# Kernel tuning notes

Hardware: AMD Instinct MI355X
Metric: run time of the kernel (lower is better)

The kernel has to match this reference:

```python
import jax, jax.numpy as jnp
import numpy as np

N_NODES = 50000
N_EDGES = 800000
D_IN = 128
D_OUT = 128
BN_EPS = 1e-5


def setup_inputs() -> dict:
    key = jax.random.key(0)
    ks = jax.random.split(key, 6)
    feat = jax.random.normal(ks[0], (N_NODES, D_IN), dtype=jnp.float32)
    src = jax.random.randint(ks[1], (N_EDGES,), 0, N_NODES, dtype=jnp.int32)
    dst = jax.random.randint(ks[2], (N_EDGES,), 0, N_NODES, dtype=jnp.int32)
    W = jax.random.normal(ks[3], (D_IN, D_OUT), dtype=jnp.float32) * (1.0 / np.sqrt(D_IN))
    b = jnp.zeros((D_OUT,), dtype=jnp.float32)
    a1 = jnp.full((1,), 0.25, dtype=jnp.float32)  # PReLU inside GraphConv
    gamma = jnp.ones((D_OUT,), dtype=jnp.float32)
    beta = jnp.zeros((D_OUT,), dtype=jnp.float32)
    a2 = jnp.full((1,), 0.25, dtype=jnp.float32)  # PReLU after BN
    return {"feat": feat, "src": src, "dst": dst, "W": W, "b": b,
            "a1": a1, "gamma": gamma, "beta": beta, "a2": a2}


def _prelu(x, a):
    return jnp.where(x >= 0, x, a * x)


def reference(feat, src, dst, W, b, a1, gamma, beta, a2):
    # Degrees (DGL clamps to min 1 to avoid inf norms)
    ones_e = jnp.ones((src.shape[0],), dtype=feat.dtype)
    out_deg = jnp.clip(jax.ops.segment_sum(ones_e, src, num_segments=N_NODES), 1.0)
    in_deg = jnp.clip(jax.ops.segment_sum(ones_e, dst, num_segments=N_NODES), 1.0)
    norm_src = jax.lax.rsqrt(out_deg)[:, None]   # [N,1]
    norm_dst = jax.lax.rsqrt(in_deg)[:, None]    # [N,1]

    # Dropout (eval mode -> identity), source normalization, projection
    h = (feat * norm_src) @ W                    # [N, D_OUT]
    # Gather-scatter neighbor aggregation (SpMM): sum over incoming edges
    msg = h[src]                                 # [E, D_OUT]
    agg = jax.ops.segment_sum(msg, dst, num_segments=N_NODES)  # [N, D_OUT]
    h = agg * norm_dst + b                       # dst normalization + bias
    h = _prelu(h, a1)                            # GraphConv activation

    # BatchNorm1d over node dimension (training-mode batch stats, biased var)
    mean = jnp.mean(h, axis=0)
    var = jnp.mean((h - mean) ** 2, axis=0)
    h = (h - mean) * jax.lax.rsqrt(var + BN_EPS) * gamma + beta

    return _prelu(h, a2)
```

## Files before the change

kernel.cpp:

```cpp
#include <hip/hip_runtime.h>
#include <hip/hip_bf16.h>

#define N_NODES 50000
#define N_EDGES 800000
#define D 128
#define BN_EPS 1e-5f
#define ELLW 64
#define PROJ_LDK 136
#define SPMM_BLOCKS 1564
#define PROJ_TILES 782

#define BINS 128
#define BIN_RANGE 391
#define BINCAP 8192
#define A_EPT 13
#define A_BLOCKS 256

typedef __attribute__((ext_vector_type(8))) short bf16x8;
typedef __attribute__((ext_vector_type(4))) float f32x4;

__device__ inline float bf_lo(unsigned u) { union { unsigned x; float f; } c; c.x = u << 16; return c.f; }
__device__ inline float bf_hi(unsigned u) { union { unsigned x; float f; } c; c.x = u & 0xffff0000u; return c.f; }
__device__ inline unsigned short f2bf(float f) {
    union { float f; unsigned u; } c; c.f = f;
    unsigned u = c.u;
    u += 0x7fff + ((u >> 16) & 1);
    return (unsigned short)(u >> 16);
}
__device__ inline unsigned cvt_pk_bf16(float lo, float hi) {
    unsigned r;
    asm("v_cvt_pk_bf16_f32 %0, %1, %2" : "=v"(r) : "v"(lo), "v"(hi));
    return r;
}

__global__ __launch_bounds__(256, 2) void bucket_proj_kernel(
        const int* __restrict__ src,
        const int* __restrict__ dst,
        int* __restrict__ gdbase,
        int* __restrict__ gsbase,
        unsigned* __restrict__ dbkt,
        unsigned short* __restrict__ sbkt,
        const float* __restrict__ feat,
        const float* __restrict__ W,
        unsigned short* __restrict__ h) {
    __shared__ int dcnt[BINS], scnt[BINS], dbase[BINS], sbase[BINS];
    __shared__ unsigned short Wt[D * PROJ_LDK];

    const int tid = threadIdx.x;

    if (blockIdx.x < A_BLOCKS) {
        if (tid < BINS) { dcnt[tid] = 0; scnt[tid] = 0; }
        __syncthreads();

        const int e0 = blockIdx.x * (256 * A_EPT) + tid;
        int s[A_EPT], t[A_EPT], dr[A_EPT], sr[A_EPT];
        #pragma unroll
        for (int k = 0; k < A_EPT; ++k) {
            int e = e0 + k * 256;
            if (e < N_EDGES) { s[k] = src[e]; t[k] = dst[e]; }
            else             { s[k] = -1;     t[k] = -1;     }
        }
        #pragma unroll
        for (int k = 0; k < A_EPT; ++k) {
            if (t[k] >= 0) dr[k] = atomicAdd(&dcnt[t[k] / BIN_RANGE], 1);
            if (s[k] >= 0) sr[k] = atomicAdd(&scnt[s[k] / BIN_RANGE], 1);
        }
        __syncthreads();
        if (tid < BINS) {
            dbase[tid] = atomicAdd(&gdbase[tid], dcnt[tid]);
            sbase[tid] = atomicAdd(&gsbase[tid], scnt[tid]);
        }
        __syncthreads();
        #pragma unroll
        for (int k = 0; k < A_EPT; ++k) {
            if (t[k] >= 0) {
                int bb = t[k] / BIN_RANGE;
                int p = dbase[bb] + dr[k];
                if (p < BINCAP)
                    dbkt[bb * BINCAP + p] = (unsigned)s[k] | ((unsigned)(t[k] - bb * BIN_RANGE) << 16);
            }
            if (s[k] >= 0) {
                int bb = s[k] / BIN_RANGE;
                int p = sbase[bb] + sr[k];
                if (p < BINCAP)
                    sbkt[bb * BINCAP + p] = (unsigned short)(s[k] - bb * BIN_RANGE);
            }
        }
    } else {
        const int tile = blockIdx.x - A_BLOCKS;
        const int wave = tid >> 6;
        const int lane = tid & 63;
        const int quad = lane >> 4;
        const int l16  = lane & 15;

        for (int idx = tid; idx < D * D; idx += 256) {
            int k = idx >> 7, d = idx & 127;
            Wt[d * PROJ_LDK + k] = f2bf(W[idx]);
        }
        __syncthreads();

        bf16x8 breg[8][4];
        #pragma unroll
        for (int dt = 0; dt < 8; ++dt)
            #pragma unroll
            for (int kk = 0; kk < 4; ++kk)
                breg[dt][kk] = *(const bf16x8*)&Wt[(dt * 16 + l16) * PROJ_LDK + kk * 32 + quad * 8];

        const int base = tile * 64;
        const int arow = base + wave * 16 + l16;
        const bool rok = arow < N_NODES;

        f32x4 acc[8];
        #pragma unroll
        for (int dt = 0; dt < 8; ++dt) acc[dt] = (f32x4){0.f, 0.f, 0.f, 0.f};

        #pragma unroll
        for (int kk = 0; kk < 4; ++kk) {
            bf16x8 af = (bf16x8){0, 0, 0, 0, 0, 0, 0, 0};
            if (rok) {
                const float4* fp = (const float4*)(feat + (size_t)arow * D + kk * 32 + quad * 8);
                float4 f0 = fp[0], f1 = fp[1];
                unsigned u0 = cvt_pk_bf16(f0.x, f0.y);
                unsigned u1 = cvt_pk_bf16(f0.z, f0.w);
                unsigned u2 = cvt_pk_bf16(f1.x, f1.y);
                unsigned u3 = cvt_pk_bf16(f1.z, f1.w);
                af[0] = (short)(u0 & 0xffff); af[1] = (short)(u0 >> 16);
                af[2] = (short)(u1 & 0xffff); af[3] = (short)(u1 >> 16);
                af[4] = (short)(u2 & 0xffff); af[5] = (short)(u2 >> 16);
                af[6] = (short)(u3 & 0xffff); af[7] = (short)(u3 >> 16);
            }
            #pragma unroll
            for (int dt = 0; dt < 8; ++dt)
                acc[dt] = __builtin_amdgcn_mfma_f32_16x16x32_bf16(af, breg[dt][kk], acc[dt], 0, 0, 0);
        }

        #pragma unroll
        for (int r = 0; r < 4; ++r) {
            int n = base + wave * 16 + quad * 4 + r;
            if (n < N_NODES) {
                unsigned short* hp = h + (size_t)n * D + l16;
                #pragma unroll
                for (int dt = 0; dt < 8; dt += 2) {
                    unsigned pk = cvt_pk_bf16(acc[dt][r], acc[dt + 1][r]);
                    hp[dt * 16]       = (unsigned short)(pk & 0xffff);
                    hp[(dt + 1) * 16] = (unsigned short)(pk >> 16);
                }
            }
        }
    }
}

__global__ __launch_bounds__(1024) void build_kernel(const int* __restrict__ gdbase,
                                                     const int* __restrict__ gsbase,
                                                     const unsigned* __restrict__ dbkt,
                                                     const unsigned short* __restrict__ sbkt,
                                                     unsigned short* __restrict__ ell,
                                                     int* __restrict__ cnt,
                                                     float* __restrict__ nsrc) {
    __shared__ int hist[BIN_RANGE];
    const int tid = threadIdx.x;
    const int bin = blockIdx.x & (BINS - 1);
    const int lo  = bin * BIN_RANGE;

    for (int i = tid; i < BIN_RANGE; i += 1024) hist[i] = 0;
    __syncthreads();

    if (blockIdx.x < BINS) {
        int count = gdbase[bin]; if (count > BINCAP) count = BINCAP;
        const unsigned* bkt = dbkt + bin * BINCAP;
        int i = tid;
        for (; i + 3072 < count; i += 4096) {
            unsigned e0 = bkt[i], e1 = bkt[i + 1024], e2 = bkt[i + 2048], e3 = bkt[i + 3072];
            int r0 = atomicAdd(&hist[e0 >> 16], 1);
            int r1 = atomicAdd(&hist[e1 >> 16], 1);
            int r2 = atomicAdd(&hist[e2 >> 16], 1);
            int r3 = atomicAdd(&hist[e3 >> 16], 1);
            if (r0 < ELLW) ell[(size_t)(lo + (e0 >> 16)) * ELLW + r0] = (unsigned short)(e0 & 0xffffu);
            if (r1 < ELLW) ell[(size_t)(lo + (e1 >> 16)) * ELLW + r1] = (unsigned short)(e1 & 0xffffu);
            if (r2 < ELLW) ell[(size_t)(lo + (e2 >> 16)) * ELLW + r2] = (unsigned short)(e2 & 0xffffu);
            if (r3 < ELLW) ell[(size_t)(lo + (e3 >> 16)) * ELLW + r3] = (unsigned short)(e3 & 0xffffu);
        }
        for (; i < count; i += 1024) {
            unsigned e = bkt[i];
            int r = atomicAdd(&hist[e >> 16], 1);
            if (r < ELLW) ell[(size_t)(lo + (e >> 16)) * ELLW + r] = (unsigned short)(e & 0xffffu);
        }
        __syncthreads();
        for (int j = tid; j < BIN_RANGE; j += 1024)
            if (lo + j < N_NODES) cnt[lo + j] = hist[j];
    } else {
        int count = gsbase[bin]; if (count > BINCAP) count = BINCAP;
        const unsigned short* bkt = sbkt + bin * BINCAP;
        int i = tid;
        for (; i + 3072 < count; i += 4096) {
            int v0 = bkt[i], v1 = bkt[i + 1024], v2 = bkt[i + 2048], v3 = bkt[i + 3072];
            atomicAdd(&hist[v0], 1); atomicAdd(&hist[v1], 1);
            atomicAdd(&hist[v2], 1); atomicAdd(&hist[v3], 1);
        }
        for (; i < count; i += 1024) atomicAdd(&hist[bkt[i]], 1);
        __syncthreads();
        for (int j = tid; j < BIN_RANGE; j += 1024)
            if (lo + j < N_NODES) {
                int dg = hist[j];
                nsrc[lo + j] = rsqrtf((float)(dg < 1 ? 1 : dg));
            }
    }
}

#define ACCA(v, ns) { accA[0] = fmaf(bf_lo((v).x), ns, accA[0]); accA[1] = fmaf(bf_hi((v).x), ns, accA[1]); \
                      accA[2] = fmaf(bf_lo((v).y), ns, accA[2]); accA[3] = fmaf(bf_hi((v).y), ns, accA[3]); \
                      accA[4] = fmaf(bf_lo((v).z), ns, accA[4]); accA[5] = fmaf(bf_hi((v).z), ns, accA[5]); \
                      accA[6] = fmaf(bf_lo((v).w), ns, accA[6]); accA[7] = fmaf(bf_hi((v).w), ns, accA[7]); }
#define ACCB(v, ns) { accB[0] = fmaf(bf_lo((v).x), ns, accB[0]); accB[1] = fmaf(bf_hi((v).x), ns, accB[1]); \
                      accB[2] = fmaf(bf_lo((v).y), ns, accB[2]); accB[3] = fmaf(bf_hi((v).y), ns, accB[3]); \
                      accB[4] = fmaf(bf_lo((v).z), ns, accB[4]); accB[5] = fmaf(bf_hi((v).z), ns, accB[5]); \
                      accB[6] = fmaf(bf_lo((v).w), ns, accB[6]); accB[7] = fmaf(bf_hi((v).w), ns, accB[7]); }
#define GA(sid) { int _s = (int)(sid); uint4 vv = *(const uint4*)(h + (size_t)_s * D + coff); \
                  float ns = nsrc[_s]; ACCA(vv, ns); }
#define GB(sid) { int _s = (int)(sid); uint4 vv = *(const uint4*)(h + (size_t)_s * D + coff); \
                  float ns = nsrc[_s]; ACCB(vv, ns); }

__global__ __launch_bounds__(256) void spmm_kernel(const int* __restrict__ cnt,
                                                   const float* __restrict__ nsrc,
                                                   const unsigned short* __restrict__ ell,
                                                   const unsigned short* __restrict__ h,
                                                   const float* __restrict__ b,
                                                   const float* __restrict__ a1,
                                                   unsigned short* __restrict__ h2,
                                                   float* __restrict__ bn_sum,
                                                   float* __restrict__ bn_sumsq) {
    const int tid  = threadIdx.x;
    const int l16  = tid & 15;
    const int slot = (blockIdx.x * 256 + tid) >> 4;
    const float alpha = a1[0];
    const size_t coff = (size_t)l16 * 8;

    float bias[8];
    #pragma unroll
    for (int j = 0; j < 8; ++j) bias[j] = b[l16 * 8 + j];

    float lsum[8] = {0,0,0,0,0,0,0,0};
    float lsq[8]  = {0,0,0,0,0,0,0,0};

    if (slot < N_NODES / 2) {
        const int n0 = slot * 2;
        const int n1 = n0 + 1;
        int dgA = cnt[n0], dgB = cnt[n1];
        int endA = (dgA < ELLW) ? dgA : ELLW;
        int endB = (dgB < ELLW) ? dgB : ELLW;
        const unsigned short* rowA = ell + (size_t)n0 * ELLW;
        const unsigned short* rowB = ell + (size_t)n1 * ELLW;

        float accA[8] = {0,0,0,0,0,0,0,0};
        float accB[8] = {0,0,0,0,0,0,0,0};
        int iA = 0, iB = 0;

        while (iA + 8 <= endA && iB + 8 <= endB) {
            uint4 ra = *(const uint4*)(rowA + iA);
            uint4 rb = *(const uint4*)(rowB + iB);
            GA(ra.x & 0xffff); GA(ra.x >> 16);
            GA(ra.y & 0xffff); GA(ra.y >> 16);
            GA(ra.z & 0xffff); GA(ra.z >> 16);
            GA(ra.w & 0xffff); GA(ra.w >> 16);
            GB(rb.x & 0xffff); GB(rb.x >> 16);
            GB(rb.y & 0xffff); GB(rb.y >> 16);
            GB(rb.z & 0xffff); GB(rb.z >> 16);
            GB(rb.w & 0xffff); GB(rb.w >> 16);
            iA += 8; iB += 8;
        }
        for (; iA + 8 <= endA; iA += 8) {
            uint4 ra = *(const uint4*)(rowA + iA);
            GA(ra.x & 0xffff); GA(ra.x >> 16);
            GA(ra.y & 0xffff); GA(ra.y >> 16);
            GA(ra.z & 0xffff); GA(ra.z >> 16);
            GA(ra.w & 0xffff); GA(ra.w >> 16);
        }
        for (; iB + 8 <= endB; iB += 8) {
            uint4 rb = *(const uint4*)(rowB + iB);
            GB(rb.x & 0xffff); GB(rb.x >> 16);
            GB(rb.y & 0xffff); GB(rb.y >> 16);
            GB(rb.z & 0xffff); GB(rb.z >> 16);
            GB(rb.w & 0xffff); GB(rb.w >> 16);
        }
        for (; iA < endA; ++iA) { GA(rowA[iA]); }
        for (; iB < endB; ++iB) { GB(rowB[iB]); }

        float ndA = rsqrtf((float)(dgA < 1 ? 1 : dgA));
        float ndB = rsqrtf((float)(dgB < 1 ? 1 : dgB));
        float xA[8], xB[8];
        #pragma unroll
        for (int j = 0; j < 8; ++j) {
            float va = accA[j] * ndA + bias[j];
            va = (va >= 0.f) ? va : alpha * va;
            xA[j] = va; lsum[j] += va; lsq[j] += va * va;
            float vb = accB[j] * ndB + bias[j];
            vb = (vb >= 0.f) ? vb : alpha * vb;
            xB[j] = vb; lsum[j] += vb; lsq[j] += vb * vb;
        }
        uint4 oA, oB;
        oA.x = cvt_pk_bf16(xA[0], xA[1]); oA.y = cvt_pk_bf16(xA[2], xA[3]);
        oA.z = cvt_pk_bf16(xA[4], xA[5]); oA.w = cvt_pk_bf16(xA[6], xA[7]);
        oB.x = cvt_pk_bf16(xB[0], xB[1]); oB.y = cvt_pk_bf16(xB[2], xB[3]);
        oB.z = cvt_pk_bf16(xB[4], xB[5]); oB.w = cvt_pk_bf16(xB[6], xB[7]);
        *(uint4*)(h2 + (size_t)n0 * D + coff) = oA;
        *(uint4*)(h2 + (size_t)n1 * D + coff) = oB;
    }

    #pragma unroll
    for (int j = 0; j < 8; ++j) {
        lsum[j] += __shfl_xor(lsum[j], 16);
        lsum[j] += __shfl_xor(lsum[j], 32);
        lsq[j]  += __shfl_xor(lsq[j], 16);
        lsq[j]  += __shfl_xor(lsq[j], 32);
    }
    __shared__ float red[4][256];
    const int wave = tid >> 6;
    const int lane = tid & 63;
    if (lane < 16) {
        #pragma unroll
        for (int j = 0; j < 8; ++j) {
            red[wave][l16 * 16 + j]     = lsum[j];
            red[wave][l16 * 16 + 8 + j] = lsq[j];
        }
    }
    __syncthreads();
    {
        float tot = red[0][tid] + red[1][tid] + red[2][tid] + red[3][tid];
        int l = tid >> 4;
        int v = tid & 15;
        int dim = l * 8 + (v & 7);
        int rep = (blockIdx.x & 3) * D;
        if (v < 8) atomicAdd(&bn_sum[rep + dim], tot);
        else       atomicAdd(&bn_sumsq[rep + dim], tot);
    }
}

__global__ __launch_bounds__(256) void final_kernel(const unsigned short* __restrict__ h2,
                                                    const float* __restrict__ bn_sum,
                                                    const float* __restrict__ bn_sumsq,
                                                    const float* __restrict__ gamma,
                                                    const float* __restrict__ beta,
                                                    const float* __restrict__ a2,
                                                    float* __restrict__ out) {
    int i8 = blockIdx.x * 256 + threadIdx.x;
    if (i8 < N_NODES * D / 8) {
        int dbase = (i8 * 8) & (D - 1);
        const float invN = 1.0f / (float)N_NODES;
        const float alpha = a2[0];
        uint4 v = ((const uint4*)h2)[i8];
        float xv[8] = { bf_lo(v.x), bf_hi(v.x), bf_lo(v.y), bf_hi(v.y),
                        bf_lo(v.z), bf_hi(v.z), bf_lo(v.w), bf_hi(v.w) };
        float r[8];
        #pragma unroll
        for (int j = 0; j < 8; ++j) {
            int d = dbase + j;
            float sm = bn_sum[d] + bn_sum[D + d] + bn_sum[2 * D + d] + bn_sum[3 * D + d];
            float sq = bn_sumsq[d] + bn_sumsq[D + d] + bn_sumsq[2 * D + d] + bn_sumsq[3 * D + d];
            float mean = sm * invN;
            float var  = sq * invN - mean * mean;
            float inv  = rsqrtf(var + BN_EPS);
            float t = (xv[j] - mean) * inv * gamma[d] + beta[d];
            r[j] = (t >= 0.f) ? t : alpha * t;
        }
        float4* po = (float4*)(out + (size_t)i8 * 8);
        po[0] = make_float4(r[0], r[1], r[2], r[3]);
        po[1] = make_float4(r[4], r[5], r[6], r[7]);
    }
}

extern "C" void kernel_launch(void* const* d_in, const int* in_sizes, int n_in,
                              void* d_out, int out_size, void* d_ws, size_t ws_size,
                              hipStream_t stream) {
    const float* feat  = (const float*)d_in[0];
    const int*   src   = (const int*)  d_in[1];
    const int*   dst   = (const int*)  d_in[2];
    const float* W     = (const float*)d_in[3];
    const float* b     = (const float*)d_in[4];
    const float* a1    = (const float*)d_in[5];
    const float* gamma = (const float*)d_in[6];
    const float* beta  = (const float*)d_in[7];
    const float* a2    = (const float*)d_in[8];
    float* out = (float*)d_out;

    char* ws = (char*)d_ws;
    int*            gdbase    = (int*)(ws + 0);
    int*            gsbase    = (int*)(ws + 512);
    float*          bn_sum    = (float*)(ws + 1024);
    float*          bn_sumsq  = (float*)(ws + 3072);
    int*            cnt       = (int*)(ws + 5120);
    float*          nsrc      = (float*)(ws + 205120);
    unsigned short* ell       = (unsigned short*)(ws + 405120);
    unsigned short* h         = (unsigned short*)(ws + 6805120);
    unsigned short* h2        = (unsigned short*)(ws + 19605120);
    unsigned*       dbkt      = (unsigned*)(ws + 32405120);
    unsigned short* sbkt      = (unsigned short*)(ws + 36599424);

    hipMemsetAsync(ws, 0, 5120, stream);

    bucket_proj_kernel<<<A_BLOCKS + PROJ_TILES, 256, 0, stream>>>(
        src, dst, gdbase, gsbase, dbkt, sbkt, feat, W, h);

    build_kernel<<<2 * BINS, 1024, 0, stream>>>(gdbase, gsbase, dbkt, sbkt,
                                                ell, cnt, nsrc);

    spmm_kernel<<<SPMM_BLOCKS, 256, 0, stream>>>(cnt, nsrc, ell, h, b, a1, h2,
                                                 bn_sum, bn_sumsq);

    final_kernel<<<(N_NODES * D / 8 + 255) / 256, 256, 0, stream>>>(h2, bn_sum, bn_sumsq,
                                                                    gamma, beta, a2, out);
}
```

Measured before the change: 179.8 us.

## Prescale projected rows by source norm in build kernel, drop per-edge nsrc gather

The source-degree normalization is now applied once per node: the build kernel's out-degree blocks rescale the bf16 projected rows of h in place. The SpMM inner loop then does plain adds with no per-edge nsrc load or multiply. All 16 gathers per iteration are issued before any accumulation to raise memory-level parallelism. This adds a read-modify-write pass over h inside build_kernel and a second bf16 rounding of h.

```diff
diff --git a/kernel.cpp b/kernel.cpp
--- a/kernel.cpp
+++ b/kernel.cpp
@@ -156,7 +156,7 @@
                                                      const unsigned short* __restrict__ sbkt,
                                                      unsigned short* __restrict__ ell,
                                                      int* __restrict__ cnt,
-                                                     float* __restrict__ nsrc) {
+                                                     unsigned short* __restrict__ h) {
     __shared__ int hist[BIN_RANGE];
     const int tid = threadIdx.x;
     const int bin = blockIdx.x & (BINS - 1);
@@ -199,29 +199,32 @@
         }
         for (; i < count; i += 1024) atomicAdd(&hist[bkt[i]], 1);
         __syncthreads();
-        for (int j = tid; j < BIN_RANGE; j += 1024)
-            if (lo + j < N_NODES) {
+        for (int idx = tid; idx < BIN_RANGE * 16; idx += 1024) {
+            int j = idx >> 4, c = idx & 15;
+            int n = lo + j;
+            if (n < N_NODES) {
                 int dg = hist[j];
-                nsrc[lo + j] = rsqrtf((float)(dg < 1 ? 1 : dg));
+                float ns = rsqrtf((float)(dg < 1 ? 1 : dg));
+                uint4* hp = (uint4*)(h + (size_t)n * D) + c;
+                uint4 v = *hp;
+                uint4 o;
+                o.x = cvt_pk_bf16(bf_lo(v.x) * ns, bf_hi(v.x) * ns);
+                o.y = cvt_pk_bf16(bf_lo(v.y) * ns, bf_hi(v.y) * ns);
+                o.z = cvt_pk_bf16(bf_lo(v.z) * ns, bf_hi(v.z) * ns);
+                o.w = cvt_pk_bf16(bf_lo(v.w) * ns, bf_hi(v.w) * ns);
+                *hp = o;
             }
-    }
-}
-
-#define ACCA(v, ns) { accA[0] = fmaf(bf_lo((v).x), ns, accA[0]); accA[1] = fmaf(bf_hi((v).x), ns, accA[1]); \
-                      accA[2] = fmaf(bf_lo((v).y), ns, accA[2]); accA[3] = fmaf(bf_hi((v).y), ns, accA[3]); \
-                      accA[4] = fmaf(bf_lo((v).z), ns, accA[4]); accA[5] = fmaf(bf_hi((v).z), ns, accA[5]); \
-                      accA[6] = fmaf(bf_lo((v).w), ns, accA[6]); accA[7] = fmaf(bf_hi((v).w), ns, accA[7]); }
-#define ACCB(v, ns) { accB[0] = fmaf(bf_lo((v).x), ns, accB[0]); accB[1] = fmaf(bf_hi((v).x), ns, accB[1]); \
-                      accB[2] = fmaf(bf_lo((v).y), ns, accB[2]); accB[3] = fmaf(bf_hi((v).y), ns, accB[3]); \
-                      accB[4] = fmaf(bf_lo((v).z), ns, accB[4]); accB[5] = fmaf(bf_hi((v).z), ns, accB[5]); \
-                      accB[6] = fmaf(bf_lo((v).w), ns, accB[6]); accB[7] = fmaf(bf_hi((v).w), ns, accB[7]); }
-#define GA(sid) { int _s = (int)(sid); uint4 vv = *(const uint4*)(h + (size_t)_s * D + coff); \
-                  float ns = nsrc[_s]; ACCA(vv, ns); }
-#define GB(sid) { int _s = (int)(sid); uint4 vv = *(const uint4*)(h + (size_t)_s * D + coff); \
-                  float ns = nsrc[_s]; ACCB(vv, ns); }
+        }
+    }
+}
+
+#define ACC8(a, v) { a[0] += bf_lo((v).x); a[1] += bf_hi((v).x); \
+                     a[2] += bf_lo((v).y); a[3] += bf_hi((v).y); \
+                     a[4] += bf_lo((v).z); a[5] += bf_hi((v).z); \
+                     a[6] += bf_lo((v).w); a[7] += bf_hi((v).w); }
+#define LDH(sid) (*(const uint4*)(h + (size_t)((sid)) * D + coff))
 
 __global__ __launch_bounds__(256) void spmm_kernel(const int* __restrict__ cnt,
-                                                   const float* __restrict__ nsrc,
                                                    const unsigned short* __restrict__ ell,
                                                    const unsigned short* __restrict__ h,
                                                    const float* __restrict__ b,
@@ -232,12 +235,7 @@
     const int tid  = threadIdx.x;
     const int l16  = tid & 15;
     const int slot = (blockIdx.x * 256 + tid) >> 4;
-    const float alpha = a1[0];
     const size_t coff = (size_t)l16 * 8;
-
-    float bias[8];
-    #pragma unroll
-    for (int j = 0; j < 8; ++j) bias[j] = b[l16 * 8 + j];
 
     float lsum[8] = {0,0,0,0,0,0,0,0};
     float lsq[8]  = {0,0,0,0,0,0,0,0};
@@ -258,32 +256,45 @@
         while (iA + 8 <= endA && iB + 8 <= endB) {
             uint4 ra = *(const uint4*)(rowA + iA);
             uint4 rb = *(const uint4*)(rowB + iB);
-            GA(ra.x & 0xffff); GA(ra.x >> 16);
-            GA(ra.y & 0xffff); GA(ra.y >> 16);
-            GA(ra.z & 0xffff); GA(ra.z >> 16);
-            GA(ra.w & 0xffff); GA(ra.w >> 16);
-            GB(rb.x & 0xffff); GB(rb.x >> 16);
-            GB(rb.y & 0xffff); GB(rb.y >> 16);
-            GB(rb.z & 0xffff); GB(rb.z >> 16);
-            GB(rb.w & 0xffff); GB(rb.w >> 16);
+            uint4 g0 = LDH(ra.x & 0xffff), g1 = LDH(ra.x >> 16);
+            uint4 g2 = LDH(ra.y & 0xffff), g3 = LDH(ra.y >> 16);
+            uint4 g4 = LDH(ra.z & 0xffff), g5 = LDH(ra.z >> 16);
+            uint4 g6 = LDH(ra.w & 0xffff), g7 = LDH(ra.w >> 16);
+            uint4 k0 = LDH(rb.x & 0xffff), k1 = LDH(rb.x >> 16);
+            uint4 k2 = LDH(rb.y & 0xffff), k3 = LDH(rb.y >> 16);
+            uint4 k4 = LDH(rb.z & 0xffff), k5 = LDH(rb.z >> 16);
+            uint4 k6 = LDH(rb.w & 0xffff), k7 = LDH(rb.w >> 16);
+            ACC8(accA, g0); ACC8(accA, g1); ACC8(accA, g2); ACC8(accA, g3);
+            ACC8(accA, g4); ACC8(accA, g5); ACC8(accA, g6); ACC8(accA, g7);
+            ACC8(accB, k0); ACC8(accB, k1); ACC8(accB, k2); ACC8(accB, k3);
+            ACC8(accB, k4); ACC8(accB, k5); ACC8(accB, k6); ACC8(accB, k7);
             iA += 8; iB += 8;
         }
         for (; iA + 8 <= endA; iA += 8) {
             uint4 ra = *(const uint4*)(rowA + iA);
-            GA(ra.x & 0xffff); GA(ra.x >> 16);
-            GA(ra.y & 0xffff); GA(ra.y >> 16);
-            GA(ra.z & 0xffff); GA(ra.z >> 16);
-            GA(ra.w & 0xffff); GA(ra.w >> 16);
+            uint4 g0 = LDH(ra.x & 0xffff), g1 = LDH(ra.x >> 16);
+            uint4 g2 = LDH(ra.y & 0xffff), g3 = LDH(ra.y >> 16);
+            uint4 g4 = LDH(ra.z & 0xffff), g5 = LDH(ra.z >> 16);
+            uint4 g6 = LDH(ra.w & 0xffff), g7 = LDH(ra.w >> 16);
+            ACC8(accA, g0); ACC8(accA, g1); ACC8(accA, g2); ACC8(accA, g3);
+            ACC8(accA, g4); ACC8(accA, g5); ACC8(accA, g6); ACC8(accA, g7);
         }
         for (; iB + 8 <= endB; iB += 8) {
             uint4 rb = *(const uint4*)(rowB + iB);
-            GB(rb.x & 0xffff); GB(rb.x >> 16);
-            GB(rb.y & 0xffff); GB(rb.y >> 16);
-            GB(rb.z & 0xffff); GB(rb.z >> 16);
-            GB(rb.w & 0xffff); GB(rb.w >> 16);
-        }
-        for (; iA < endA; ++iA) { GA(rowA[iA]); }
-        for (; iB < endB; ++iB) { GB(rowB[iB]); }
+            uint4 k0 = LDH(rb.x & 0xffff), k1 = LDH(rb.x >> 16);
+            uint4 k2 = LDH(rb.y & 0xffff), k3 = LDH(rb.y >> 16);
+            uint4 k4 = LDH(rb.z & 0xffff), k5 = LDH(rb.z >> 16);
+            uint4 k6 = LDH(rb.w & 0xffff), k7 = LDH(rb.w >> 16);
+            ACC8(accB, k0); ACC8(accB, k1); ACC8(accB, k2); ACC8(accB, k3);
+            ACC8(accB, k4); ACC8(accB, k5); ACC8(accB, k6); ACC8(accB, k7);
+        }
+        for (; iA < endA; ++iA) { uint4 g = LDH(rowA[iA]); ACC8(accA, g); }
+        for (; iB < endB; ++iB) { uint4 k = LDH(rowB[iB]); ACC8(accB, k); }
+
+        const float alpha = a1[0];
+        float bias[8];
+        #pragma unroll
+        for (int j = 0; j < 8; ++j) bias[j] = b[l16 * 8 + j];
 
         float ndA = rsqrtf((float)(dgA < 1 ? 1 : dgA));
         float ndB = rsqrtf((float)(dgB < 1 ? 1 : dgB));
@@ -388,7 +399,6 @@
     float*          bn_sum    = (float*)(ws + 1024);
     float*          bn_sumsq  = (float*)(ws + 3072);
     int*            cnt       = (int*)(ws + 5120);
-    float*          nsrc      = (float*)(ws + 205120);
     unsigned short* ell       = (unsigned short*)(ws + 405120);
     unsigned short* h         = (unsigned short*)(ws + 6805120);
     unsigned short* h2        = (unsigned short*)(ws + 19605120);
@@ -401,9 +411,9 @@
         src, dst, gdbase, gsbase, dbkt, sbkt, feat, W, h);
 
     build_kernel<<<2 * BINS, 1024, 0, stream>>>(gdbase, gsbase, dbkt, sbkt,
-                                                ell, cnt, nsrc);
-
-    spmm_kernel<<<SPMM_BLOCKS, 256, 0, stream>>>(cnt, nsrc, ell, h, b, a1, h2,
+                                                ell, cnt, h);
+
+    spmm_kernel<<<SPMM_BLOCKS, 256, 0, stream>>>(cnt, ell, h, b, a1, h2,
                                                  bn_sum, bn_sumsq);
 
     final_kernel<<<(N_NODES * D / 8 + 255) / 256, 256, 0, stream>>>(h2, bn_sum, bn_sumsq,
```

New measurement: 176.8 us. No clear change (-1.6%).
